# Optimization experiments

Hardware: AMD Instinct MI355X
Metric: run time of the kernel (lower is better)

Reference implementation:

```python
import jax, jax.numpy as jnp
import numpy as np

N, E = 100000, 1600000
IN, HID, HEADS, OUT = 128, 16, 4, 64
SLOPE = 0.2  # leaky_relu negative_slope default


def setup_inputs() -> dict:
    key = jax.random.key(0)
    ks = jax.random.split(key, 12)
    s = 0.1  # xavier-ish scale
    return {
        "x": jax.random.normal(ks[0], (N, IN), jnp.float32),
        "edge_index": jax.random.randint(ks[1], (2, E), 0, N, jnp.int32),
        "W1": jax.random.normal(ks[2], (IN, HEADS * HID), jnp.float32) * s,
        "att_l1": jax.random.normal(ks[3], (1, HEADS, HID), jnp.float32) * s,
        "att_r1": jax.random.normal(ks[4], (1, HEADS, HID), jnp.float32) * s,
        "res_W1": jax.random.normal(ks[5], (IN, HEADS * HID), jnp.float32) * s,
        "b1": jnp.zeros((HEADS * HID,), jnp.float32),
        "W2": jax.random.normal(ks[6], (HEADS * HID, OUT), jnp.float32) * s,
        "att_l2": jax.random.normal(ks[7], (1, 1, OUT), jnp.float32) * s,
        "att_r2": jax.random.normal(ks[8], (1, 1, OUT), jnp.float32) * s,
        "b2": jnp.zeros((OUT,), jnp.float32),
    }


def agdn_conv(x, W, att_l, att_r, bias, res_W, src, dst):
    # x: [n, in]; W: [in, H*C]; att_*: [1, H, C]
    n = x.shape[0]
    H, C = att_l.shape[1], att_l.shape[2]
    x_lin = (x @ W).reshape(n, H, C)
    # residual: res_fc if present, else identity on x_lin (residual=True path)
    x_res = (x @ res_W) if res_W is not None else x_lin.reshape(n, H * C)
    al = jnp.sum(x_lin * att_l, axis=-1)  # [n, H]
    ar = jnp.sum(x_lin * att_r, axis=-1)  # [n, H]
    logits = jax.nn.leaky_relu(al[src] + ar[dst], SLOPE)  # [E, H]
    # segment softmax over incoming edges of each dst node
    m = jax.ops.segment_max(logits, dst, num_segments=n)
    e = jnp.exp(logits - m[dst])
    ssum = jax.ops.segment_sum(e, dst, num_segments=n)
    alpha = e / (ssum[dst] + 1e-16)  # [E, H]
    msg = x_lin[src] * alpha[:, :, None]  # [E, H, C]
    out = jax.ops.segment_sum(msg, dst, num_segments=n).reshape(n, H * C)
    return out + x_res + bias


def reference(x, edge_index, W1, att_l1, att_r1, res_W1, b1, W2, att_l2, att_r2, b2):
    src, dst = edge_index[0], edge_index[1]
    h = agdn_conv(x, W1, att_l1, att_r1, b1, res_W1, src, dst)
    h = jax.nn.elu(h)
    # last layer: heads=1, in==heads*out so res_fc is None (residual = x_lin)
    return agdn_conv(h, W2, att_l2, att_r2, b2, None, src, dst)
```

## Files before the change

### kernel.cpp

```cpp
#include <hip/hip_runtime.h>
#include <hip/hip_bf16.h>
#include <hip/hip_fp16.h>
#include <math.h>

#define NN 100000
#define EE 1600000
#define IN_DIM 128
#define HID 16
#define HEADS 4
#define D1 64
#define OUT_DIM 64
#define SLOPE 0.2f

#define NB 391
#define BCAP 5120
#define BINA_CHUNK 4096
#define BINA_BLOCKS ((EE + BINA_CHUNK - 1) / BINA_CHUNK)
#define NODE_BLOCKS ((NN + 63) / 64)
#define AGG_BLOCKS (NN / 32)

#define W1COLS 144
#define LDB1 272
#define LDB2 144

typedef __attribute__((ext_vector_type(8))) short bf16x8;
typedef __attribute__((ext_vector_type(4))) float f32x4;

__device__ __forceinline__ float leaky(float v) { return v > 0.f ? v : SLOPE * v; }
__device__ __forceinline__ unsigned short f2bf(float f) {
    __hip_bfloat16 h = __float2bfloat16(f);
    return *(unsigned short*)&h;
}
__device__ __forceinline__ __half2 u2h2(unsigned u) {
    union { unsigned u; __half2 h; } c; c.u = u; return c.h;
}
__device__ __forceinline__ bf16x8 pack8(float4 a, float4 b) {
    bf16x8 r;
    r[0] = (short)f2bf(a.x); r[1] = (short)f2bf(a.y);
    r[2] = (short)f2bf(a.z); r[3] = (short)f2bf(a.w);
    r[4] = (short)f2bf(b.x); r[5] = (short)f2bf(b.y);
    r[6] = (short)f2bf(b.z); r[7] = (short)f2bf(b.w);
    return r;
}

__global__ __launch_bounds__(256, 4) void node1_kernel(
        const float* __restrict__ x,
        const unsigned short* __restrict__ Wtb,
        const float* __restrict__ b1,
        __half* __restrict__ xlin1h,
        __half* __restrict__ acc1h,
        float* __restrict__ al1,
        float* __restrict__ ar1) {
    __shared__ char smemB[W1COLS * LDB1];
    int t = threadIdx.x;
    int base = blockIdx.x * 64;
    int wave = t >> 6, lane = t & 63;
    int quad = lane >> 4, li = lane & 15;
    int node = base + wave * 16 + li;

    uint4 breg[9];
#pragma unroll
    for (int s = 0; s < 9; s++) {
        int seg = s * 256 + t;
        breg[s] = *(const uint4*)(Wtb + (seg >> 4) * 128 + (seg & 15) * 8);
    }
    float4 xreg[8];
#pragma unroll
    for (int i = 0; i < 8; i++) xreg[i] = make_float4(0.f, 0.f, 0.f, 0.f);
    if (node < NN) {
        const float* xp = x + (size_t)node * IN_DIM + quad * 8;
#pragma unroll
        for (int kc = 0; kc < 4; kc++) {
            xreg[kc * 2]     = *(const float4*)(xp + kc * 32);
            xreg[kc * 2 + 1] = *(const float4*)(xp + kc * 32 + 4);
        }
    }
#pragma unroll
    for (int s = 0; s < 9; s++) {
        int seg = s * 256 + t;
        *(uint4*)(smemB + (seg >> 4) * LDB1 + (seg & 15) * 16) = breg[s];
    }
    __syncthreads();

    f32x4 accs[9];
#pragma unroll
    for (int nt = 0; nt < 9; nt++) accs[nt] = (f32x4){0.f, 0.f, 0.f, 0.f};
#pragma unroll
    for (int kc = 0; kc < 4; kc++) {
        bf16x8 afrag = pack8(xreg[kc * 2], xreg[kc * 2 + 1]);
        const char* brow = smemB + kc * 64 + quad * 16;
#pragma unroll
        for (int nt = 0; nt < 9; nt++) {
            bf16x8 bfrag = *(const bf16x8*)(brow + (nt * 16 + li) * LDB1);
            accs[nt] = __builtin_amdgcn_mfma_f32_16x16x32_bf16(afrag, bfrag, accs[nt], 0, 0, 0);
        }
    }

    int m0 = base + wave * 16;
#pragma unroll
    for (int nt = 0; nt < 4; nt++) {
#pragma unroll
        for (int j = 0; j < 4; j++) {
            int nd = m0 + quad * 4 + j;
            if (nd < NN) xlin1h[(size_t)nd * D1 + nt * 16 + li] = __float2half(accs[nt][j]);
        }
    }
#pragma unroll
    for (int nt = 4; nt < 8; nt++) {
        int col = (nt - 4) * 16 + li;
        float bv = b1[col];
#pragma unroll
        for (int j = 0; j < 4; j++) {
            int nd = m0 + quad * 4 + j;
            if (nd < NN) acc1h[(size_t)nd * D1 + col] = __float2half(accs[nt][j] + bv);
        }
    }
#pragma unroll
    for (int j = 0; j < 4; j++) {
        int nd = m0 + quad * 4 + j;
        if (nd < NN) {
            if (li < 4) al1[nd * HEADS + li] = accs[8][j];
            else if (li < 8) ar1[nd * HEADS + (li - 4)] = accs[8][j];
        }
    }
}

__global__ void prep_kernel(int* __restrict__ bucket_cursor,
                            const float* __restrict__ W1,
                            const float* __restrict__ resW,
                            const float* __restrict__ W2,
                            const float* __restrict__ attl1,
                            const float* __restrict__ attr1,
                            const float* __restrict__ attl2,
                            const float* __restrict__ attr2,
                            unsigned short* __restrict__ Wtb,
                            unsigned short* __restrict__ W2tb,
                            float* __restrict__ vl, float* __restrict__ vr) {
    int t = threadIdx.x;
    if (blockIdx.x == 0) {
        if (t < NB) bucket_cursor[t] = t * BCAP;
    } else if (blockIdx.x == 1) {
        for (int idx = t; idx < W1COLS * 128; idx += 512) {
            int col = idx >> 7, k = idx & 127;
            float w = 0.f;
            if (col < 64) {
                w = W1[k * 64 + col];
            } else if (col < 128) {
                w = resW[k * 64 + (col - 64)];
            } else if (col < 132) {
                int hh = col - 128;
                for (int c = 0; c < HID; c++)
                    w += W1[k * 64 + hh * HID + c] * attl1[hh * HID + c];
            } else if (col < 136) {
                int hh = col - 132;
                for (int c = 0; c < HID; c++)
                    w += W1[k * 64 + hh * HID + c] * attr1[hh * HID + c];
            }
            Wtb[idx] = f2bf(w);
        }
    } else {
        for (int idx = t; idx < 64 * 64; idx += 512) {
            int col = idx >> 6, k = idx & 63;
            W2tb[idx] = f2bf(W2[k * 64 + col]);
        }
        if (t < D1) {
            float a = 0.f, b = 0.f;
            for (int o = 0; o < OUT_DIM; o++) {
                float w = W2[t * OUT_DIM + o];
                a += w * attl2[o];
                b += w * attr2[o];
            }
            vl[t] = a; vr[t] = b;
        }
    }
}

__global__ __launch_bounds__(256) void binA_kernel(const int* __restrict__ src,
                                                   const int* __restrict__ dst,
                                                   int* __restrict__ bucket_cursor,
                                                   unsigned* __restrict__ binned) {
    __shared__ unsigned spack[BINA_CHUNK];
    __shared__ unsigned short sbkt[BINA_CHUNK];
    __shared__ int lhist[512], lscan[512], gbase[512], lcur[512];
    int t = threadIdx.x;
    lhist[t] = 0; lhist[t + 256] = 0;
    lcur[t] = 0;  lcur[t + 256] = 0;
    __syncthreads();
    int e0 = blockIdx.x * BINA_CHUNK;
    int nvalid = EE - e0; if (nvalid > BINA_CHUNK) nvalid = BINA_CHUNK;
    unsigned pk[16];
    unsigned short bk[16];
#pragma unroll
    for (int i = 0; i < 16; i++) {
        int e = e0 + t + i * 256;
        if (e < EE) {
            int d = dst[e], s = src[e];
            int b = d >> 8;
            pk[i] = ((unsigned)(d & 255) << 24) | (unsigned)s;
            bk[i] = (unsigned short)b;
            atomicAdd(&lhist[b], 1);
        } else bk[i] = 0xFFFFu;
    }
    __syncthreads();
    int c1 = lhist[t], c2 = lhist[t + 256];
    for (int off = 1; off < 512; off <<= 1) {
        int a1 = (t >= off) ? lhist[t - off] : 0;
        int a2 = (t + 256 >= off) ? lhist[t + 256 - off] : 0;
        __syncthreads();
        lhist[t] += a1; lhist[t + 256] += a2;
        __syncthreads();
    }
    lscan[t] = lhist[t] - c1;
    lscan[t + 256] = lhist[t + 256] - c2;
    if (c1) gbase[t] = atomicAdd(&bucket_cursor[t], c1);
    if (c2) gbase[t + 256] = atomicAdd(&bucket_cursor[t + 256], c2);
    __syncthreads();
#pragma unroll
    for (int i = 0; i < 16; i++) {
        if (bk[i] != 0xFFFFu) {
            int b = bk[i];
            int pos = atomicAdd(&lcur[b], 1);
            int slot = lscan[b] + pos;
            spack[slot] = pk[i];
            sbkt[slot] = (unsigned short)b;
        }
    }
    __syncthreads();
    for (int j = t; j < nvalid; j += 256) {
        int b = sbkt[j];
        int idx = gbase[b] + (j - lscan[b]);
        if (idx < (b + 1) * BCAP) binned[idx] = spack[j];
    }
}

__global__ __launch_bounds__(256) void binB_kernel(const unsigned* __restrict__ binned,
                                                   const int* __restrict__ bucket_cursor,
                                                   int* __restrict__ row_ptr,
                                                   int* __restrict__ counts,
                                                   int* __restrict__ sorted_src) {
    __shared__ int lcount[256], lrow[256], lcur[256];
    int b = blockIdx.x, t = threadIdx.x;
    int start = b * BCAP;
    int cnt = bucket_cursor[b] - start;
    if (cnt > BCAP) cnt = BCAP;
    lcount[t] = 0;
    __syncthreads();
    for (int i = t; i < cnt; i += 256) {
        atomicAdd(&lcount[binned[start + i] >> 24], 1);
    }
    __syncthreads();
    int v = lcount[t];
    lrow[t] = v;
    __syncthreads();
    for (int off = 1; off < 256; off <<= 1) {
        int a = (t >= off) ? lrow[t - off] : 0;
        __syncthreads();
        lrow[t] += a;
        __syncthreads();
    }
    int ex = lrow[t] - v;
    __syncthreads();
    lrow[t] = ex;
    lcur[t] = 0;
    int node = (b << 8) + t;
    if (node < NN) {
        row_ptr[node] = start + ex;
        counts[node] = v;
    }
    __syncthreads();
    for (int i = t; i < cnt; i += 256) {
        unsigned p = binned[start + i];
        int low = p >> 24;
        int pos = atomicAdd(&lcur[low], 1);
        sorted_src[start + lrow[low] + pos] = (int)(p & 0xFFFFFFu);
    }
}

__global__ __launch_bounds__(256) void agg1_kernel(
        const int* __restrict__ sorted_src, const int* __restrict__ row_ptr,
        const int* __restrict__ counts,
        const float* __restrict__ al1, const float* __restrict__ ar1,
        const __half* __restrict__ xlin1h, const __half* __restrict__ acc1h,
        unsigned short* __restrict__ hb,
        const float* __restrict__ vl, const float* __restrict__ vr,
        float* __restrict__ al2, float* __restrict__ ar2) {
    __shared__ __half s_alpha[4][8][65][4];
    __shared__ int    s_src[4][8][65];
    int w = threadIdx.x >> 6, lane = threadIdx.x & 63;
    int g = lane >> 3, li = lane & 7;
    int d = blockIdx.x * 32 + w * 8 + g;
    int rs = row_ptr[d];
    int deg = counts[d];
    const float4 arv = *(const float4*)(ar1 + d * 4);
    int h = li >> 1;

    int maxdeg = deg;
    maxdeg = max(maxdeg, __shfl_xor(maxdeg, 8, 64));
    maxdeg = max(maxdeg, __shfl_xor(maxdeg, 16, 64));
    maxdeg = max(maxdeg, __shfl_xor(maxdeg, 32, 64));
    bool big = maxdeg > 64;

    float s0 = 0.f, s1 = 0.f, s2 = 0.f, s3 = 0.f;
    if (!big) {
#pragma unroll
        for (int it = 0; it < 8; it++) {
            int e = li + it * 8;
            if (e < deg) {
                int s = sorted_src[rs + e];
                const float4 alv = *(const float4*)(al1 + s * 4);
                float e0 = __expf(leaky(alv.x + arv.x));
                float e1 = __expf(leaky(alv.y + arv.y));
                float e2 = __expf(leaky(alv.z + arv.z));
                float e3 = __expf(leaky(alv.w + arv.w));
                s0 += e0; s1 += e1; s2 += e2; s3 += e3;
                __half2 h01 = __floats2half2_rn(e0, e1);
                __half2 h23 = __floats2half2_rn(e2, e3);
                *(uint2*)&s_alpha[w][g][e][0] =
                    make_uint2(*(unsigned*)&h01, *(unsigned*)&h23);
                s_src[w][g][e] = s;
            }
        }
    } else {
        for (int e = li; e < deg; e += 8) {
            int s = sorted_src[rs + e];
            const float4 alv = *(const float4*)(al1 + s * 4);
            s0 += __expf(leaky(alv.x + arv.x));
            s1 += __expf(leaky(alv.y + arv.y));
            s2 += __expf(leaky(alv.z + arv.z));
            s3 += __expf(leaky(alv.w + arv.w));
        }
    }
#pragma unroll
    for (int off = 1; off < 8; off <<= 1) {
        s0 += __shfl_xor(s0, off, 64);
        s1 += __shfl_xor(s1, off, 64);
        s2 += __shfl_xor(s2, off, 64);
        s3 += __shfl_xor(s3, off, 64);
    }
    float inv0 = 0.f, inv1 = 0.f, inv2 = 0.f, inv3 = 0.f;
    if (deg > 0) {
        inv0 = 1.f / (s0 + 1e-16f); inv1 = 1.f / (s1 + 1e-16f);
        inv2 = 1.f / (s2 + 1e-16f); inv3 = 1.f / (s3 + 1e-16f);
    }
    float invh = (h == 0) ? inv0 : (h == 1) ? inv1 : (h == 2) ? inv2 : inv3;
    __half2 invh2 = __floats2half2_rn(invh, invh);

    __half2 a01 = __floats2half2_rn(0.f, 0.f);
    __half2 a23 = a01, a45 = a01, a67 = a01;
    float fb0=0.f, fb1=0.f, fb2=0.f, fb3=0.f, fb4=0.f, fb5=0.f, fb6=0.f, fb7=0.f;
    if (!big) {
        for (int i0 = 0; i0 < maxdeg; i0 += 4) {
            int ss[4]; __half ah[4]; uint4 uu[4];
#pragma unroll
            for (int j = 0; j < 4; j++) {
                int i = i0 + j;
                ah[j] = __float2half(0.f);
                ss[j] = 0;
                if (i < deg) { ss[j] = s_src[w][g][i]; ah[j] = s_alpha[w][g][i][h]; }
            }
#pragma unroll
            for (int j = 0; j < 4; j++) {
                int i = i0 + j;
                uu[j] = make_uint4(0u, 0u, 0u, 0u);
                if (i < deg) uu[j] = *(const uint4*)(xlin1h + (size_t)ss[j] * D1 + li * 8);
            }
#pragma unroll
            for (int j = 0; j < 4; j++) {
                __half2 a2 = __hmul2(__half2half2(ah[j]), invh2);
                a01 = __hfma2(a2, u2h2(uu[j].x), a01);
                a23 = __hfma2(a2, u2h2(uu[j].y), a23);
                a45 = __hfma2(a2, u2h2(uu[j].z), a45);
                a67 = __hfma2(a2, u2h2(uu[j].w), a67);
            }
        }
    } else {
        float arh = (h == 0) ? arv.x : (h == 1) ? arv.y : (h == 2) ? arv.z : arv.w;
        for (int i = 0; i < deg; i++) {
            int s = sorted_src[rs + i];
            const float4 alv = *(const float4*)(al1 + s * 4);
            float lv = (h == 0) ? alv.x : (h == 1) ? alv.y : (h == 2) ? alv.z : alv.w;
            float a = __expf(leaky(lv + arh)) * invh;
            uint4 u = *(const uint4*)(xlin1h + (size_t)s * D1 + li * 8);
            float2 x01 = __half22float2(u2h2(u.x));
            float2 x23 = __half22float2(u2h2(u.y));
            float2 x45 = __half22float2(u2h2(u.z));
            float2 x67 = __half22float2(u2h2(u.w));
            fb0 += a * x01.x; fb1 += a * x01.y; fb2 += a * x23.x; fb3 += a * x23.y;
            fb4 += a * x45.x; fb5 += a * x45.y; fb6 += a * x67.x; fb7 += a * x67.y;
        }
    }
    float c0, c1, c2, c3, c4, c5, c6, c7;
    { float2 tv;
      tv = __half22float2(a01); c0 = tv.x + fb0; c1 = tv.y + fb1;
      tv = __half22float2(a23); c2 = tv.x + fb2; c3 = tv.y + fb3;
      tv = __half22float2(a45); c4 = tv.x + fb4; c5 = tv.y + fb5;
      tv = __half22float2(a67); c6 = tv.x + fb6; c7 = tv.y + fb7; }
    uint4 rres = *(const uint4*)(acc1h + (size_t)d * D1 + li * 8);
    { float2 tv;
      tv = __half22float2(u2h2(rres.x)); c0 += tv.x; c1 += tv.y;
      tv = __half22float2(u2h2(rres.y)); c2 += tv.x; c3 += tv.y;
      tv = __half22float2(u2h2(rres.z)); c4 += tv.x; c5 += tv.y;
      tv = __half22float2(u2h2(rres.w)); c6 += tv.x; c7 += tv.y; }
    c0 = c0 > 0.f ? c0 : (__expf(c0) - 1.f);
    c1 = c1 > 0.f ? c1 : (__expf(c1) - 1.f);
    c2 = c2 > 0.f ? c2 : (__expf(c2) - 1.f);
    c3 = c3 > 0.f ? c3 : (__expf(c3) - 1.f);
    c4 = c4 > 0.f ? c4 : (__expf(c4) - 1.f);
    c5 = c5 > 0.f ? c5 : (__expf(c5) - 1.f);
    c6 = c6 > 0.f ? c6 : (__expf(c6) - 1.f);
    c7 = c7 > 0.f ? c7 : (__expf(c7) - 1.f);
    union { unsigned short us[8]; uint4 u4; } hw;
    hw.us[0] = f2bf(c0); hw.us[1] = f2bf(c1); hw.us[2] = f2bf(c2); hw.us[3] = f2bf(c3);
    hw.us[4] = f2bf(c4); hw.us[5] = f2bf(c5); hw.us[6] = f2bf(c6); hw.us[7] = f2bf(c7);
    *(uint4*)(hb + (size_t)d * D1 + li * 8) = hw.u4;
    const float4 vla = *(const float4*)(vl + li * 8);
    const float4 vlb = *(const float4*)(vl + li * 8 + 4);
    const float4 vra = *(const float4*)(vr + li * 8);
    const float4 vrb = *(const float4*)(vr + li * 8 + 4);
    float pl = c0 * vla.x + c1 * vla.y + c2 * vla.z + c3 * vla.w
             + c4 * vlb.x + c5 * vlb.y + c6 * vlb.z + c7 * vlb.w;
    float pr = c0 * vra.x + c1 * vra.y + c2 * vra.z + c3 * vra.w
             + c4 * vrb.x + c5 * vrb.y + c6 * vrb.z + c7 * vrb.w;
#pragma unroll
    for (int off = 1; off < 8; off <<= 1) {
        pl += __shfl_xor(pl, off, 64);
        pr += __shfl_xor(pr, off, 64);
    }
    if (li == 0) { al2[d] = pl; ar2[d] = pr; }
}

__global__ __launch_bounds__(256) void node2_kernel(
        const unsigned short* __restrict__ hb,
        const unsigned short* __restrict__ W2tb,
        __half* __restrict__ xlin2h) {
    __shared__ char smemB[64 * LDB2];
    int t = threadIdx.x;
    int base = blockIdx.x * 64;
    int wave = t >> 6, lane = t & 63;
    int quad = lane >> 4, li = lane & 15;
    int node = base + wave * 16 + li;

    uint4 breg[2];
#pragma unroll
    for (int s = 0; s < 2; s++) {
        int seg = s * 256 + t;
        breg[s] = *(const uint4*)(W2tb + (seg >> 3) * 64 + (seg & 7) * 8);
    }
    bf16x8 afr[2];
#pragma unroll
    for (int kc = 0; kc < 2; kc++)
#pragma unroll
        for (int i = 0; i < 8; i++) afr[kc][i] = 0;
    if (node < NN) {
        afr[0] = *(const bf16x8*)(hb + (size_t)node * D1 + quad * 8);
        afr[1] = *(const bf16x8*)(hb + (size_t)node * D1 + 32 + quad * 8);
    }
#pragma unroll
    for (int s = 0; s < 2; s++) {
        int seg = s * 256 + t;
        *(uint4*)(smemB + (seg >> 3) * LDB2 + (seg & 7) * 16) = breg[s];
    }
    __syncthreads();

    f32x4 accs[4];
#pragma unroll
    for (int nt = 0; nt < 4; nt++) accs[nt] = (f32x4){0.f, 0.f, 0.f, 0.f};
#pragma unroll
    for (int kc = 0; kc < 2; kc++) {
        const char* brow = smemB + kc * 64 + quad * 16;
#pragma unroll
        for (int nt = 0; nt < 4; nt++) {
            bf16x8 bfrag = *(const bf16x8*)(brow + (nt * 16 + li) * LDB2);
            accs[nt] = __builtin_amdgcn_mfma_f32_16x16x32_bf16(afr[kc], bfrag, accs[nt], 0, 0, 0);
        }
    }

    int m0 = base + wave * 16;
#pragma unroll
    for (int nt = 0; nt < 4; nt++) {
        int col = nt * 16 + li;
#pragma unroll
        for (int j = 0; j < 4; j++) {
            int nd = m0 + quad * 4 + j;
            if (nd < NN) xlin2h[(size_t)nd * OUT_DIM + col] = __float2half(accs[nt][j]);
        }
    }
}

__global__ __launch_bounds__(256) void agg2_kernel(
        const int* __restrict__ sorted_src, const int* __restrict__ row_ptr,
        const int* __restrict__ counts,
        const float* __restrict__ al2, const float* __restrict__ ar2,
        const __half* __restrict__ xlin2h, const float* __restrict__ b2,
        float* __restrict__ out) {
    __shared__ __half s_alpha[4][8][65];
    __shared__ int    s_src[4][8][65];
    int w = threadIdx.x >> 6, lane = threadIdx.x & 63;
    int g = lane >> 3, li = lane & 7;
    int d = blockIdx.x * 32 + w * 8 + g;
    int rs = row_ptr[d];
    int deg = counts[d];
    float ard = ar2[d];

    int maxdeg = deg;
    maxdeg = max(maxdeg, __shfl_xor(maxdeg, 8, 64));
    maxdeg = max(maxdeg, __shfl_xor(maxdeg, 16, 64));
    maxdeg = max(maxdeg, __shfl_xor(maxdeg, 32, 64));
    bool big = maxdeg > 64;

    float ssum = 0.f;
    if (!big) {
#pragma unroll
        for (int it = 0; it < 8; it++) {
            int e = li + it * 8;
            if (e < deg) {
                int s = sorted_src[rs + e];
                float ex = __expf(leaky(al2[s] + ard));
                ssum += ex;
                s_alpha[w][g][e] = __float2half(ex);
                s_src[w][g][e] = s;
            }
        }
    } else {
        for (int e = li; e < deg; e += 8) {
            int s = sorted_src[rs + e];
            ssum += __expf(leaky(al2[s] + ard));
        }
    }
#pragma unroll
    for (int off = 1; off < 8; off <<= 1) ssum += __shfl_xor(ssum, off, 64);
    float inv = (deg > 0) ? 1.f / (ssum + 1e-16f) : 0.f;
    __half2 inv2h = __floats2half2_rn(inv, inv);

    __half2 a01 = __floats2half2_rn(0.f, 0.f);
    __half2 a23 = a01, a45 = a01, a67 = a01;
    float fb0=0.f, fb1=0.f, fb2=0.f, fb3=0.f, fb4=0.f, fb5=0.f, fb6=0.f, fb7=0.f;
    if (!big) {
        for (int i0 = 0; i0 < maxdeg; i0 += 4) {
            int ss[4]; __half ah[4]; uint4 uu[4];
#pragma unroll
            for (int j = 0; j < 4; j++) {
                int i = i0 + j;
                ah[j] = __float2half(0.f);
                ss[j] = 0;
                if (i < deg) { ss[j] = s_src[w][g][i]; ah[j] = s_alpha[w][g][i]; }
            }
#pragma unroll
            for (int j = 0; j < 4; j++) {
                int i = i0 + j;
                uu[j] = make_uint4(0u, 0u, 0u, 0u);
                if (i < deg) uu[j] = *(const uint4*)(xlin2h + (size_t)ss[j] * OUT_DIM + li * 8);
            }
#pragma unroll
            for (int j = 0; j < 4; j++) {
                __half2 a2 = __hmul2(__half2half2(ah[j]), inv2h);
                a01 = __hfma2(a2, u2h2(uu[j].x), a01);
                a23 = __hfma2(a2, u2h2(uu[j].y), a23);
                a45 = __hfma2(a2, u2h2(uu[j].z), a45);
                a67 = __hfma2(a2, u2h2(uu[j].w), a67);
            }
        }
    } else {
        for (int i = 0; i < deg; i++) {
            int s = sorted_src[rs + i];
            float a = __expf(leaky(al2[s] + ard)) * inv;
            uint4 u = *(const uint4*)(xlin2h + (size_t)s * OUT_DIM + li * 8);
            float2 x01 = __half22float2(u2h2(u.x));
            float2 x23 = __half22float2(u2h2(u.y));
            float2 x45 = __half22float2(u2h2(u.z));
            float2 x67 = __half22float2(u2h2(u.w));
            fb0 += a * x01.x; fb1 += a * x01.y; fb2 += a * x23.x; fb3 += a * x23.y;
            fb4 += a * x45.x; fb5 += a * x45.y; fb6 += a * x67.x; fb7 += a * x67.y;
        }
    }
    float c0, c1, c2, c3, c4, c5, c6, c7;
    { float2 tv;
      tv = __half22float2(a01); c0 = tv.x + fb0; c1 = tv.y + fb1;
      tv = __half22float2(a23); c2 = tv.x + fb2; c3 = tv.y + fb3;
      tv = __half22float2(a45); c4 = tv.x + fb4; c5 = tv.y + fb5;
      tv = __half22float2(a67); c6 = tv.x + fb6; c7 = tv.y + fb7; }
    uint4 own = *(const uint4*)(xlin2h + (size_t)d * OUT_DIM + li * 8);
    { float2 tv;
      tv = __half22float2(u2h2(own.x)); c0 += tv.x; c1 += tv.y;
      tv = __half22float2(u2h2(own.y)); c2 += tv.x; c3 += tv.y;
      tv = __half22float2(u2h2(own.z)); c4 += tv.x; c5 += tv.y;
      tv = __half22float2(u2h2(own.w)); c6 += tv.x; c7 += tv.y; }
    const float4 bva = *(const float4*)(b2 + li * 8);
    const float4 bvb = *(const float4*)(b2 + li * 8 + 4);
    c0 += bva.x; c1 += bva.y; c2 += bva.z; c3 += bva.w;
    c4 += bvb.x; c5 += bvb.y; c6 += bvb.z; c7 += bvb.w;
    float* p = out + (size_t)d * OUT_DIM + li * 8;
    *(float4*)p = make_float4(c0, c1, c2, c3);
    *(float4*)(p + 4) = make_float4(c4, c5, c6, c7);
}

extern "C" void kernel_launch(void* const* d_in, const int* in_sizes, int n_in,
                              void* d_out, int out_size, void* d_ws, size_t ws_size,
                              hipStream_t stream) {
    const float* x     = (const float*)d_in[0];
    const int*   eidx  = (const int*)d_in[1];
    const float* W1    = (const float*)d_in[2];
    const float* attl1 = (const float*)d_in[3];
    const float* attr1 = (const float*)d_in[4];
    const float* resW1 = (const float*)d_in[5];
    const float* b1    = (const float*)d_in[6];
    const float* W2    = (const float*)d_in[7];
    const float* attl2 = (const float*)d_in[8];
    const float* attr2 = (const float*)d_in[9];
    const float* b2    = (const float*)d_in[10];

    const int* src = eidx;
    const int* dst = eidx + EE;

    __half* xlin1h = (__half*)d_ws;
    __half* acc1h  = xlin1h + (size_t)NN * D1;
    unsigned short* hb = (unsigned short*)(acc1h + (size_t)NN * D1);
    float* al1   = (float*)(hb + (size_t)NN * D1);
    float* ar1   = al1 + (size_t)NN * HEADS;
    float* al2   = ar1 + (size_t)NN * HEADS;
    float* ar2   = al2 + NN;
    float* vl    = ar2 + NN;
    float* vr    = vl + D1;
    unsigned short* Wtb  = (unsigned short*)(vr + D1);
    unsigned short* W2tb = Wtb + W1COLS * 128;
    int* counts        = (int*)(W2tb + 64 * 64);
    int* row_ptr       = counts + NN;
    int* bucket_cursor = row_ptr + NN;
    int* sorted_src    = bucket_cursor + 512;
    unsigned* binned = (unsigned*)d_out;
    __half* xlin2h = xlin1h;

    float* out = (float*)d_out;

    prep_kernel<<<3, 512, 0, stream>>>(bucket_cursor, W1, resW1, W2,
                                       attl1, attr1, attl2, attr2,
                                       Wtb, W2tb, vl, vr);
    binA_kernel<<<BINA_BLOCKS, 256, 0, stream>>>(src, dst, bucket_cursor, binned);
    node1_kernel<<<NODE_BLOCKS, 256, 0, stream>>>(x, Wtb, b1,
                                                  xlin1h, acc1h, al1, ar1);
    binB_kernel<<<NB, 256, 0, stream>>>(binned, bucket_cursor,
                                        row_ptr, counts, sorted_src);

    agg1_kernel<<<AGG_BLOCKS, 256, 0, stream>>>(sorted_src, row_ptr, counts,
                                                al1, ar1, xlin1h, acc1h, hb,
                                                vl, vr, al2, ar2);

    node2_kernel<<<NODE_BLOCKS, 256, 0, stream>>>(hb, W2tb, xlin2h);
    agg2_kernel<<<AGG_BLOCKS, 256, 0, stream>>>(sorted_src, row_ptr, counts,
                                                al2, ar2, xlin2h, b2, out);
}
```

Measured before the change: 258.1 us.

## Sort nodes by degree class, fuse binning with node1 GEMM, widen gather unroll

Adds a degree-class histogram in binB plus scan and scatter kernels that build a permutation of nodes grouped by in-degree. Both aggregation kernels then process nodes in that order, so the 8 nodes sharing a wave have similar degrees and less work is lost to divergence on maxdeg. The edge-binning and node1 GEMM kernels are merged into one launch that branches on block index, so the two independent stages can run at the same time. The gather loops are unrolled from 4 to 8 to keep more loads in flight. The cost is two extra small launches, an extra permutation load per node, and scattered writes for hb/out.

```diff
diff --git a/kernel.cpp b/kernel.cpp
--- a/kernel.cpp
+++ b/kernel.cpp
@@ -18,6 +18,8 @@
 #define BINA_BLOCKS ((EE + BINA_CHUNK - 1) / BINA_CHUNK)
 #define NODE_BLOCKS ((NN + 63) / 64)
 #define AGG_BLOCKS (NN / 32)
+#define SCAT_BLOCKS ((NN + 1023) / 1024)
+#define NCLS 32
 
 #define W1COLS 144
 #define LDB1 272
@@ -43,89 +45,8 @@
     return r;
 }
 
-__global__ __launch_bounds__(256, 4) void node1_kernel(
-        const float* __restrict__ x,
-        const unsigned short* __restrict__ Wtb,
-        const float* __restrict__ b1,
-        __half* __restrict__ xlin1h,
-        __half* __restrict__ acc1h,
-        float* __restrict__ al1,
-        float* __restrict__ ar1) {
-    __shared__ char smemB[W1COLS * LDB1];
-    int t = threadIdx.x;
-    int base = blockIdx.x * 64;
-    int wave = t >> 6, lane = t & 63;
-    int quad = lane >> 4, li = lane & 15;
-    int node = base + wave * 16 + li;
-
-    uint4 breg[9];
-#pragma unroll
-    for (int s = 0; s < 9; s++) {
-        int seg = s * 256 + t;
-        breg[s] = *(const uint4*)(Wtb + (seg >> 4) * 128 + (seg & 15) * 8);
-    }
-    float4 xreg[8];
-#pragma unroll
-    for (int i = 0; i < 8; i++) xreg[i] = make_float4(0.f, 0.f, 0.f, 0.f);
-    if (node < NN) {
-        const float* xp = x + (size_t)node * IN_DIM + quad * 8;
-#pragma unroll
-        for (int kc = 0; kc < 4; kc++) {
-            xreg[kc * 2]     = *(const float4*)(xp + kc * 32);
-            xreg[kc * 2 + 1] = *(const float4*)(xp + kc * 32 + 4);
-        }
-    }
-#pragma unroll
-    for (int s = 0; s < 9; s++) {
-        int seg = s * 256 + t;
-        *(uint4*)(smemB + (seg >> 4) * LDB1 + (seg & 15) * 16) = breg[s];
-    }
-    __syncthreads();
-
-    f32x4 accs[9];
-#pragma unroll
-    for (int nt = 0; nt < 9; nt++) accs[nt] = (f32x4){0.f, 0.f, 0.f, 0.f};
-#pragma unroll
-    for (int kc = 0; kc < 4; kc++) {
-        bf16x8 afrag = pack8(xreg[kc * 2], xreg[kc * 2 + 1]);
-        const char* brow = smemB + kc * 64 + quad * 16;
-#pragma unroll
-        for (int nt = 0; nt < 9; nt++) {
-            bf16x8 bfrag = *(const bf16x8*)(brow + (nt * 16 + li) * LDB1);
-            accs[nt] = __builtin_amdgcn_mfma_f32_16x16x32_bf16(afrag, bfrag, accs[nt], 0, 0, 0);
-        }
-    }
-
-    int m0 = base + wave * 16;
-#pragma unroll
-    for (int nt = 0; nt < 4; nt++) {
-#pragma unroll
-        for (int j = 0; j < 4; j++) {
-            int nd = m0 + quad * 4 + j;
-            if (nd < NN) xlin1h[(size_t)nd * D1 + nt * 16 + li] = __float2half(accs[nt][j]);
-        }
-    }
-#pragma unroll
-    for (int nt = 4; nt < 8; nt++) {
-        int col = (nt - 4) * 16 + li;
-        float bv = b1[col];
-#pragma unroll
-        for (int j = 0; j < 4; j++) {
-            int nd = m0 + quad * 4 + j;
-            if (nd < NN) acc1h[(size_t)nd * D1 + col] = __float2half(accs[nt][j] + bv);
-        }
-    }
-#pragma unroll
-    for (int j = 0; j < 4; j++) {
-        int nd = m0 + quad * 4 + j;
-        if (nd < NN) {
-            if (li < 4) al1[nd * HEADS + li] = accs[8][j];
-            else if (li < 8) ar1[nd * HEADS + (li - 4)] = accs[8][j];
-        }
-    }
-}
-
 __global__ void prep_kernel(int* __restrict__ bucket_cursor,
+                            int* __restrict__ cls_cnt,
                             const float* __restrict__ W1,
                             const float* __restrict__ resW,
                             const float* __restrict__ W2,
@@ -139,6 +60,7 @@
     int t = threadIdx.x;
     if (blockIdx.x == 0) {
         if (t < NB) bucket_cursor[t] = t * BCAP;
+        if (t < NCLS) cls_cnt[t] = 0;
     } else if (blockIdx.x == 1) {
         for (int idx = t; idx < W1COLS * 128; idx += 512) {
             int col = idx >> 7, k = idx & 127;
@@ -175,18 +97,20 @@
     }
 }
 
-__global__ __launch_bounds__(256) void binA_kernel(const int* __restrict__ src,
-                                                   const int* __restrict__ dst,
-                                                   int* __restrict__ bucket_cursor,
-                                                   unsigned* __restrict__ binned) {
-    __shared__ unsigned spack[BINA_CHUNK];
-    __shared__ unsigned short sbkt[BINA_CHUNK];
-    __shared__ int lhist[512], lscan[512], gbase[512], lcur[512];
+__device__ __forceinline__ void binA_body(char* smem, int bid,
+        const int* __restrict__ src, const int* __restrict__ dst,
+        int* __restrict__ bucket_cursor, unsigned* __restrict__ binned) {
+    unsigned* spack = (unsigned*)smem;
+    unsigned short* sbkt = (unsigned short*)(smem + 16384);
+    int* lhist = (int*)(smem + 24576);
+    int* lscan = lhist + 512;
+    int* gbase = lscan + 512;
+    int* lcur  = gbase + 512;
     int t = threadIdx.x;
     lhist[t] = 0; lhist[t + 256] = 0;
     lcur[t] = 0;  lcur[t + 256] = 0;
     __syncthreads();
-    int e0 = blockIdx.x * BINA_CHUNK;
+    int e0 = bid * BINA_CHUNK;
     int nvalid = EE - e0; if (nvalid > BINA_CHUNK) nvalid = BINA_CHUNK;
     unsigned pk[16];
     unsigned short bk[16];
@@ -233,17 +157,112 @@
     }
 }
 
+__device__ __forceinline__ void node1_body(char* smemB, int bid,
+        const float* __restrict__ x, const unsigned short* __restrict__ Wtb,
+        const float* __restrict__ b1, __half* __restrict__ xlin1h,
+        __half* __restrict__ acc1h, float* __restrict__ al1,
+        float* __restrict__ ar1) {
+    int t = threadIdx.x;
+    int base = bid * 64;
+    int wave = t >> 6, lane = t & 63;
+    int quad = lane >> 4, li = lane & 15;
+    int node = base + wave * 16 + li;
+
+    uint4 breg[9];
+#pragma unroll
+    for (int s = 0; s < 9; s++) {
+        int seg = s * 256 + t;
+        breg[s] = *(const uint4*)(Wtb + (seg >> 4) * 128 + (seg & 15) * 8);
+    }
+    float4 xreg[8];
+#pragma unroll
+    for (int i = 0; i < 8; i++) xreg[i] = make_float4(0.f, 0.f, 0.f, 0.f);
+    if (node < NN) {
+        const float* xp = x + (size_t)node * IN_DIM + quad * 8;
+#pragma unroll
+        for (int kc = 0; kc < 4; kc++) {
+            xreg[kc * 2]     = *(const float4*)(xp + kc * 32);
+            xreg[kc * 2 + 1] = *(const float4*)(xp + kc * 32 + 4);
+        }
+    }
+#pragma unroll
+    for (int s = 0; s < 9; s++) {
+        int seg = s * 256 + t;
+        *(uint4*)(smemB + (seg >> 4) * LDB1 + (seg & 15) * 16) = breg[s];
+    }
+    __syncthreads();
+
+    f32x4 accs[9];
+#pragma unroll
+    for (int nt = 0; nt < 9; nt++) accs[nt] = (f32x4){0.f, 0.f, 0.f, 0.f};
+#pragma unroll
+    for (int kc = 0; kc < 4; kc++) {
+        bf16x8 afrag = pack8(xreg[kc * 2], xreg[kc * 2 + 1]);
+        const char* brow = smemB + kc * 64 + quad * 16;
+#pragma unroll
+        for (int nt = 0; nt < 9; nt++) {
+            bf16x8 bfrag = *(const bf16x8*)(brow + (nt * 16 + li) * LDB1);
+            accs[nt] = __builtin_amdgcn_mfma_f32_16x16x32_bf16(afrag, bfrag, accs[nt], 0, 0, 0);
+        }
+    }
+
+    int m0 = base + wave * 16;
+#pragma unroll
+    for (int nt = 0; nt < 4; nt++) {
+#pragma unroll
+        for (int j = 0; j < 4; j++) {
+            int nd = m0 + quad * 4 + j;
+            if (nd < NN) xlin1h[(size_t)nd * D1 + nt * 16 + li] = __float2half(accs[nt][j]);
+        }
+    }
+#pragma unroll
+    for (int nt = 4; nt < 8; nt++) {
+        int col = (nt - 4) * 16 + li;
+        float bv = b1[col];
+#pragma unroll
+        for (int j = 0; j < 4; j++) {
+            int nd = m0 + quad * 4 + j;
+            if (nd < NN) acc1h[(size_t)nd * D1 + col] = __float2half(accs[nt][j] + bv);
+        }
+    }
+#pragma unroll
+    for (int j = 0; j < 4; j++) {
+        int nd = m0 + quad * 4 + j;
+        if (nd < NN) {
+            if (li < 4) al1[nd * HEADS + li] = accs[8][j];
+            else if (li < 8) ar1[nd * HEADS + (li - 4)] = accs[8][j];
+        }
+    }
+}
+
+__global__ __launch_bounds__(256, 4) void fusedA_kernel(
+        const int* __restrict__ src, const int* __restrict__ dst,
+        int* __restrict__ bucket_cursor, unsigned* __restrict__ binned,
+        const float* __restrict__ x, const unsigned short* __restrict__ Wtb,
+        const float* __restrict__ b1, __half* __restrict__ xlin1h,
+        __half* __restrict__ acc1h, float* __restrict__ al1,
+        float* __restrict__ ar1) {
+    __shared__ __align__(16) char smem[W1COLS * LDB1];
+    if (blockIdx.x < BINA_BLOCKS)
+        binA_body(smem, blockIdx.x, src, dst, bucket_cursor, binned);
+    else
+        node1_body(smem, blockIdx.x - BINA_BLOCKS, x, Wtb, b1, xlin1h, acc1h, al1, ar1);
+}
+
 __global__ __launch_bounds__(256) void binB_kernel(const unsigned* __restrict__ binned,
                                                    const int* __restrict__ bucket_cursor,
                                                    int* __restrict__ row_ptr,
                                                    int* __restrict__ counts,
-                                                   int* __restrict__ sorted_src) {
+                                                   int* __restrict__ sorted_src,
+                                                   int* __restrict__ cls_cnt) {
     __shared__ int lcount[256], lrow[256], lcur[256];
+    __shared__ int lcls[NCLS];
     int b = blockIdx.x, t = threadIdx.x;
     int start = b * BCAP;
     int cnt = bucket_cursor[b] - start;
     if (cnt > BCAP) cnt = BCAP;
     lcount[t] = 0;
+    if (t < NCLS) lcls[t] = 0;
     __syncthreads();
     for (int i = t; i < cnt; i += 256) {
         atomicAdd(&lcount[binned[start + i] >> 24], 1);
@@ -266,8 +285,10 @@
     if (node < NN) {
         row_ptr[node] = start + ex;
         counts[node] = v;
-    }
-    __syncthreads();
+        atomicAdd(&lcls[min(v >> 1, NCLS - 1)], 1);
+    }
+    __syncthreads();
+    if (t < NCLS && lcls[t]) atomicAdd(&cls_cnt[t], lcls[t]);
     for (int i = t; i < cnt; i += 256) {
         unsigned p = binned[start + i];
         int low = p >> 24;
@@ -276,7 +297,49 @@
     }
 }
 
+__global__ void scan_kernel(const int* __restrict__ cls_cnt,
+                            int* __restrict__ cls_cur) {
+    if (threadIdx.x == 0) {
+        int run = 0;
+        for (int i = 0; i < NCLS; i++) {
+            cls_cur[i] = run;
+            run += cls_cnt[i];
+        }
+    }
+}
+
+__global__ __launch_bounds__(256) void scatter_kernel(const int* __restrict__ counts,
+                                                      int* __restrict__ cls_cur,
+                                                      int* __restrict__ perm) {
+    __shared__ int lhist[NCLS], lbase[NCLS], lcur[NCLS];
+    int t = threadIdx.x;
+    if (t < NCLS) { lhist[t] = 0; lcur[t] = 0; }
+    __syncthreads();
+    int cls[4];
+#pragma unroll
+    for (int j = 0; j < 4; j++) {
+        int node = blockIdx.x * 1024 + j * 256 + t;
+        cls[j] = -1;
+        if (node < NN) {
+            cls[j] = min(counts[node] >> 1, NCLS - 1);
+            atomicAdd(&lhist[cls[j]], 1);
+        }
+    }
+    __syncthreads();
+    if (t < NCLS && lhist[t]) lbase[t] = atomicAdd(&cls_cur[t], lhist[t]);
+    __syncthreads();
+#pragma unroll
+    for (int j = 0; j < 4; j++) {
+        int node = blockIdx.x * 1024 + j * 256 + t;
+        if (node < NN) {
+            int pos = lbase[cls[j]] + atomicAdd(&lcur[cls[j]], 1);
+            perm[pos] = node;
+        }
+    }
+}
+
 __global__ __launch_bounds__(256) void agg1_kernel(
+        const int* __restrict__ perm,
         const int* __restrict__ sorted_src, const int* __restrict__ row_ptr,
         const int* __restrict__ counts,
         const float* __restrict__ al1, const float* __restrict__ ar1,
@@ -288,7 +351,7 @@
     __shared__ int    s_src[4][8][65];
     int w = threadIdx.x >> 6, lane = threadIdx.x & 63;
     int g = lane >> 3, li = lane & 7;
-    int d = blockIdx.x * 32 + w * 8 + g;
+    int d = perm[blockIdx.x * 32 + w * 8 + g];
     int rs = row_ptr[d];
     int deg = counts[d];
     const float4 arv = *(const float4*)(ar1 + d * 4);
@@ -302,16 +365,16 @@
 
     float s0 = 0.f, s1 = 0.f, s2 = 0.f, s3 = 0.f;
     if (!big) {
-#pragma unroll
-        for (int it = 0; it < 8; it++) {
-            int e = li + it * 8;
-            if (e < deg) {
-                int s = sorted_src[rs + e];
-                const float4 alv = *(const float4*)(al1 + s * 4);
-                float e0 = __expf(leaky(alv.x + arv.x));
-                float e1 = __expf(leaky(alv.y + arv.y));
-                float e2 = __expf(leaky(alv.z + arv.z));
-                float e3 = __expf(leaky(alv.w + arv.w));
+        for (int e = li; e < maxdeg; e += 8) {
+            bool v = e < deg;
+            int s = v ? sorted_src[rs + e] : 0;
+            float4 alv = make_float4(0.f, 0.f, 0.f, 0.f);
+            if (v) alv = *(const float4*)(al1 + s * 4);
+            float e0 = __expf(leaky(alv.x + arv.x));
+            float e1 = __expf(leaky(alv.y + arv.y));
+            float e2 = __expf(leaky(alv.z + arv.z));
+            float e3 = __expf(leaky(alv.w + arv.w));
+            if (v) {
                 s0 += e0; s1 += e1; s2 += e2; s3 += e3;
                 __half2 h01 = __floats2half2_rn(e0, e1);
                 __half2 h23 = __floats2half2_rn(e2, e3);
@@ -349,23 +412,23 @@
     __half2 a23 = a01, a45 = a01, a67 = a01;
     float fb0=0.f, fb1=0.f, fb2=0.f, fb3=0.f, fb4=0.f, fb5=0.f, fb6=0.f, fb7=0.f;
     if (!big) {
-        for (int i0 = 0; i0 < maxdeg; i0 += 4) {
-            int ss[4]; __half ah[4]; uint4 uu[4];
-#pragma unroll
-            for (int j = 0; j < 4; j++) {
+        for (int i0 = 0; i0 < maxdeg; i0 += 8) {
+            int ss[8]; __half ah[8]; uint4 uu[8];
+#pragma unroll
+            for (int j = 0; j < 8; j++) {
                 int i = i0 + j;
-                ah[j] = __float2half(0.f);
-                ss[j] = 0;
-                if (i < deg) { ss[j] = s_src[w][g][i]; ah[j] = s_alpha[w][g][i][h]; }
-            }
-#pragma unroll
-            for (int j = 0; j < 4; j++) {
+                bool v = i < deg;
+                ss[j] = v ? s_src[w][g][i] : 0;
+                ah[j] = v ? s_alpha[w][g][i][h] : __float2half(0.f);
+            }
+#pragma unroll
+            for (int j = 0; j < 8; j++) {
                 int i = i0 + j;
                 uu[j] = make_uint4(0u, 0u, 0u, 0u);
                 if (i < deg) uu[j] = *(const uint4*)(xlin1h + (size_t)ss[j] * D1 + li * 8);
             }
 #pragma unroll
-            for (int j = 0; j < 4; j++) {
+            for (int j = 0; j < 8; j++) {
                 __half2 a2 = __hmul2(__half2half2(ah[j]), invh2);
                 a01 = __hfma2(a2, u2h2(uu[j].x), a01);
                 a23 = __hfma2(a2, u2h2(uu[j].y), a23);
@@ -488,6 +551,7 @@
 }
 
 __global__ __launch_bounds__(256) void agg2_kernel(
+        const int* __restrict__ perm,
         const int* __restrict__ sorted_src, const int* __restrict__ row_ptr,
         const int* __restrict__ counts,
         const float* __restrict__ al2, const float* __restrict__ ar2,
@@ -497,7 +561,7 @@
     __shared__ int    s_src[4][8][65];
     int w = threadIdx.x >> 6, lane = threadIdx.x & 63;
     int g = lane >> 3, li = lane & 7;
-    int d = blockIdx.x * 32 + w * 8 + g;
+    int d = perm[blockIdx.x * 32 + w * 8 + g];
     int rs = row_ptr[d];
     int deg = counts[d];
     float ard = ar2[d];
@@ -510,12 +574,12 @@
 
     float ssum = 0.f;
     if (!big) {
-#pragma unroll
-        for (int it = 0; it < 8; it++) {
-            int e = li + it * 8;
-            if (e < deg) {
-                int s = sorted_src[rs + e];
-                float ex = __expf(leaky(al2[s] + ard));
+        for (int e = li; e < maxdeg; e += 8) {
+            bool v = e < deg;
+            int s = v ? sorted_src[rs + e] : 0;
+            float lv = v ? al2[s] : 0.f;
+            float ex = __expf(leaky(lv + ard));
+            if (v) {
                 ssum += ex;
                 s_alpha[w][g][e] = __float2half(ex);
                 s_src[w][g][e] = s;
@@ -536,23 +600,23 @@
     __half2 a23 = a01, a45 = a01, a67 = a01;
     float fb0=0.f, fb1=0.f, fb2=0.f, fb3=0.f, fb4=0.f, fb5=0.f, fb6=0.f, fb7=0.f;
     if (!big) {
-        for (int i0 = 0; i0 < maxdeg; i0 += 4) {
-            int ss[4]; __half ah[4]; uint4 uu[4];
-#pragma unroll
-            for (int j = 0; j < 4; j++) {
+        for (int i0 = 0; i0 < maxdeg; i0 += 8) {
+            int ss[8]; __half ah[8]; uint4 uu[8];
+#pragma unroll
+            for (int j = 0; j < 8; j++) {
                 int i = i0 + j;
-                ah[j] = __float2half(0.f);
-                ss[j] = 0;
-                if (i < deg) { ss[j] = s_src[w][g][i]; ah[j] = s_alpha[w][g][i]; }
-            }
-#pragma unroll
-            for (int j = 0; j < 4; j++) {
+                bool v = i < deg;
+                ss[j] = v ? s_src[w][g][i] : 0;
+                ah[j] = v ? s_alpha[w][g][i] : __float2half(0.f);
+            }
+#pragma unroll
+            for (int j = 0; j < 8; j++) {
                 int i = i0 + j;
                 uu[j] = make_uint4(0u, 0u, 0u, 0u);
                 if (i < deg) uu[j] = *(const uint4*)(xlin2h + (size_t)ss[j] * OUT_DIM + li * 8);
             }
 #pragma unroll
-            for (int j = 0; j < 4; j++) {
+            for (int j = 0; j < 8; j++) {
                 __half2 a2 = __hmul2(__half2half2(ah[j]), inv2h);
                 a01 = __hfma2(a2, u2h2(uu[j].x), a01);
                 a23 = __hfma2(a2, u2h2(uu[j].y), a23);
@@ -626,26 +690,31 @@
     int* counts        = (int*)(W2tb + 64 * 64);
     int* row_ptr       = counts + NN;
     int* bucket_cursor = row_ptr + NN;
-    int* sorted_src    = bucket_cursor + 512;
+    int* cls_cnt       = bucket_cursor + 512;
+    int* cls_cur       = cls_cnt + NCLS;
+    int* perm          = cls_cur + NCLS;
+    int* sorted_src    = perm + NN;
     unsigned* binned = (unsigned*)d_out;
     __half* xlin2h = xlin1h;
 
     float* out = (float*)d_out;
 
-    prep_kernel<<<3, 512, 0, stream>>>(bucket_cursor, W1, resW1, W2,
+    prep_kernel<<<3, 512, 0, stream>>>(bucket_cursor, cls_cnt, W1, resW1, W2,
                                        attl1, attr1, attl2, attr2,
                                        Wtb, W2tb, vl, vr);
-    binA_kernel<<<BINA_BLOCKS, 256, 0, stream>>>(src, dst, bucket_cursor, binned);
-    node1_kernel<<<NODE_BLOCKS, 256, 0, stream>>>(x, Wtb, b1,
-                                                  xlin1h, acc1h, al1, ar1);
+    fusedA_kernel<<<BINA_BLOCKS + NODE_BLOCKS, 256, 0, stream>>>(
+        src, dst, bucket_cursor, binned,
+        x, Wtb, b1, xlin1h, acc1h, al1, ar1);
     binB_kernel<<<NB, 256, 0, stream>>>(binned, bucket_cursor,
-                                        row_ptr, counts, sorted_src);
-
-    agg1_kernel<<<AGG_BLOCKS, 256, 0, stream>>>(sorted_src, row_ptr, counts,
+                                        row_ptr, counts, sorted_src, cls_cnt);
+    scan_kernel<<<1, 64, 0, stream>>>(cls_cnt, cls_cur);
+    scatter_kernel<<<SCAT_BLOCKS, 256, 0, stream>>>(counts, cls_cur, perm);
+
+    agg1_kernel<<<AGG_BLOCKS, 256, 0, stream>>>(perm, sorted_src, row_ptr, counts,
                                                 al1, ar1, xlin1h, acc1h, hb,
                                                 vl, vr, al2, ar2);
 
     node2_kernel<<<NODE_BLOCKS, 256, 0, stream>>>(hb, W2tb, xlin2h);
-    agg2_kernel<<<AGG_BLOCKS, 256, 0, stream>>>(sorted_src, row_ptr, counts,
+    agg2_kernel<<<AGG_BLOCKS, 256, 0, stream>>>(perm, sorted_src, row_ptr, counts,
                                                 al2, ar2, xlin2h, b2, out);
 }
```

Result: slower. 264.1 us (+2.3%).
